# Kernel tuning notes

Measured on AMD Instinct MI355X. Metric: run time of the kernel, lower is better.

The kernel has to match this reference:

```python
import jax, jax.numpy as jnp
import numpy as np

A, C, H, W = 8, 256, 80, 108      # agents, channels, cf_h, cf_w from the module
NUM_CLASSES = 7
OUT_H, OUT_W = 256, 256


def warp_affine(feat, M):
    """Bilinear affine warp of feat [C,H,W] with sampling matrix M [2,3].
    dst(u,v) = src(M @ [u,v,1]); out-of-bounds samples are zero (kornia zero padding)."""
    c, h, w = feat.shape
    vs, us = jnp.meshgrid(jnp.arange(h, dtype=feat.dtype),
                          jnp.arange(w, dtype=feat.dtype), indexing='ij')
    sx = M[0, 0] * us + M[0, 1] * vs + M[0, 2]
    sy = M[1, 0] * us + M[1, 1] * vs + M[1, 2]
    x0 = jnp.floor(sx)
    y0 = jnp.floor(sy)
    wx = sx - x0
    wy = sy - y0
    x0i = x0.astype(jnp.int32)
    y0i = y0.astype(jnp.int32)

    def tap(yy, xx, wgt):
        valid = (yy >= 0) & (yy < h) & (xx >= 0) & (xx < w)
        yyc = jnp.clip(yy, 0, h - 1)
        xxc = jnp.clip(xx, 0, w - 1)
        return feat[:, yyc, xxc] * (wgt * valid)[None]

    return (tap(y0i, x0i, (1 - wy) * (1 - wx))
            + tap(y0i, x0i + 1, (1 - wy) * wx)
            + tap(y0i + 1, x0i, wy * (1 - wx))
            + tap(y0i + 1, x0i + 1, wy * wx))


def resize_bilinear_align_corners(img, oh, ow):
    """F.interpolate(..., mode='bilinear', align_corners=True) for img [N,C,H,W]."""
    h, w = img.shape[-2:]
    ys = jnp.linspace(0.0, h - 1.0, oh, dtype=img.dtype)
    xs = jnp.linspace(0.0, w - 1.0, ow, dtype=img.dtype)
    y0 = jnp.clip(jnp.floor(ys).astype(jnp.int32), 0, h - 2)
    x0 = jnp.clip(jnp.floor(xs).astype(jnp.int32), 0, w - 2)
    wy = (ys - y0)[None, None, :, None]
    wx = (xs - x0)[None, None, None, :]
    row = img[:, :, y0, :] * (1 - wy) + img[:, :, y0 + 1, :] * wy   # [N,C,oh,W]
    return row[:, :, :, x0] * (1 - wx) + row[:, :, :, x0 + 1] * wx  # [N,C,oh,ow]


def setup_inputs() -> dict:
    key = jax.random.key(0)
    k1, k2, k3, k4, k5, k6 = jax.random.split(key, 6)
    x = jax.random.normal(k1, (A, C, H, W), jnp.float32)
    # near-identity per-pair affine sampling matrices with small rotation/shear + translation
    rel = jnp.tile(jnp.eye(2, 3, dtype=jnp.float32), (A, A, 1, 1))
    rel = rel + 0.05 * jax.random.normal(k2, (A, A, 2, 3), jnp.float32)
    rel = rel.at[..., 2].add(10.0 * jax.random.normal(k3, (A, A, 2), jnp.float32))
    adjacency_matrix = jax.random.randint(k4, (A, A), 0, 2, dtype=jnp.int32)
    car_masks = jax.random.uniform(k5, (A, 256, 256), jnp.float32)
    w_cls = 0.02 * jax.random.normal(k6, (NUM_CLASSES, C), jnp.float32)
    b_cls = jnp.zeros((NUM_CLASSES,), jnp.float32)
    return {"x": x, "relative_tfs": rel, "adjacency_matrix": adjacency_matrix,
            "car_masks": car_masks, "w_cls": w_cls, "b_cls": b_cls}


def reference(x, relative_tfs, adjacency_matrix, car_masks, w_cls, b_cls):
    # x = x + F.interpolate(car_masks.unsqueeze(1), (cf_h, cf_w), 'bilinear')  (align_corners=False)
    cm = jax.image.resize(car_masks[:, None], (A, 1, H, W), method="bilinear")
    x = x + cm

    # aggregate_features: per ego-agent i, warp all agents' features into i's frame,
    # zero agents with adjacency[i,j]==0, and sum over j.
    warp_all = jax.vmap(warp_affine)                       # over agents j
    warped = jax.vmap(lambda Ms: warp_all(x, Ms))(relative_tfs)  # [A,A,C,H,W]
    fov = (adjacency_matrix != 0).astype(x.dtype)          # [A,A]
    aggr = jnp.einsum('ij,ijchw->ichw', fov, warped)       # masked sum over j

    def predict(f):  # mask_prediction (1x1 conv) + sigmoid
        logits = jnp.einsum('oc,achw->aohw', w_cls, f) + b_cls[None, :, None, None]
        return jax.nn.sigmoid(logits)

    solo_x = resize_bilinear_align_corners(predict(x), OUT_H, OUT_W)
    aggr_x = resize_bilinear_align_corners(predict(aggr), OUT_H, OUT_W)
    return (solo_x, aggr_x)
```

## Files before the change

kernel.cpp:

```cpp
#include <hip/hip_runtime.h>
#include <hip/hip_bf16.h>

#define A_N 8
#define C_N 256
#define H_N 80
#define W_N 108
#define P_N (H_N * W_N)
#define P4_N (P_N / 4)
#define O_N 7
#define MH 256
#define MW 256
#define OUT_HW 256
#define TPA 34

__device__ __forceinline__ float sigmoidf_(float zv) {
    return 1.0f / (1.0f + __expf(-zv));
}

__launch_bounds__(256)
__global__ void k_conv(const float* __restrict__ x, const float* __restrict__ masks,
                       const float* __restrict__ w, const float* __restrict__ b,
                       float* __restrict__ z, float* __restrict__ ssolo)
{
    __shared__ float4 s_red[4][64][O_N];
    __shared__ float  s_cm[256];

    const int tid = threadIdx.x;
    const int bi  = blockIdx.x;
    const int a   = bi / TPA;
    const int t   = bi - a * TPA;

    {
        const int ppx = t * 256 + tid;
        const int pc  = min(ppx, P_N - 1);
        const int oy = pc / W_N, ox = pc - oy * W_N;
        const float ksy = 256.0f / 80.0f;
        const float ksx = 256.0f / 108.0f;
        const float rky = 0.3125f;
        const float rkx = 0.421875f;
        const float sfy = ((float)oy + 0.5f) * ksy - 0.5f;
        const float sfx = ((float)ox + 0.5f) * ksx - 0.5f;
        const int iyS = (int)ceilf(sfy - ksy);
        const int ixS = (int)ceilf(sfx - ksx);

        float wxv[5];
        float wxs = 0.0f;
        #pragma unroll
        for (int q = 0; q < 5; ++q) {
            const int ix = ixS + q;
            float wv = fmaxf(0.0f, 1.0f - fabsf(sfx - (float)ix) * rkx);
            wv = (ix >= 0 && ix < MW) ? wv : 0.0f;
            wxv[q] = wv;
            wxs += wv;
        }
        const float* mp = masks + (size_t)a * (MH * MW);
        float acc = 0.0f, wys = 0.0f;
        #pragma unroll
        for (int r = 0; r < 7; ++r) {
            const int iy = iyS + r;
            float wy = fmaxf(0.0f, 1.0f - fabsf(sfy - (float)iy) * rky);
            wy = (iy >= 0 && iy < MH) ? wy : 0.0f;
            wys += wy;
            const float* row = mp + min(max(iy, 0), MH - 1) * MW;
            float rs = 0.0f;
            #pragma unroll
            for (int q = 0; q < 5; ++q)
                rs = fmaf(wxv[q], row[min(max(ixS + q, 0), MW - 1)], rs);
            acc = fmaf(wy, rs, acc);
        }
        s_cm[tid] = acc / (wys * wxs);
    }
    __syncthreads();

    const int wq   = tid >> 6;
    const int lane = tid & 63;
    const int px4  = t * 64 + lane;
    const int px4c = min(px4, P4_N - 1);

    const float4 cm4 = make_float4(s_cm[lane * 4], s_cm[lane * 4 + 1],
                                   s_cm[lane * 4 + 2], s_cm[lane * 4 + 3]);

    const float4* xp = reinterpret_cast<const float4*>(x)
                     + (size_t)(a * C_N + wq * 64) * P4_N + px4c;
    const float* wp = w + wq * 64;

    float4 acc[O_N];
    #pragma unroll
    for (int o = 0; o < O_N; ++o) acc[o] = make_float4(0.f, 0.f, 0.f, 0.f);

    float4 va[8], vb[8];

#define LOADB(buf, cb)                                            \
    _Pragma("unroll")                                             \
    for (int u = 0; u < 8; ++u) buf[u] = xp[(size_t)((cb) + u) * P4_N];

#define COMPB(buf, cb)                                            \
    _Pragma("unroll")                                             \
    for (int u = 0; u < 8; ++u) {                                 \
        float4 v = buf[u];                                        \
        v.x += cm4.x; v.y += cm4.y; v.z += cm4.z; v.w += cm4.w;   \
        _Pragma("unroll")                                         \
        for (int o = 0; o < O_N; ++o) {                           \
            const float wv = wp[o * C_N + (cb) + u];              \
            acc[o].x = fmaf(wv, v.x, acc[o].x);                   \
            acc[o].y = fmaf(wv, v.y, acc[o].y);                   \
            acc[o].z = fmaf(wv, v.z, acc[o].z);                   \
            acc[o].w = fmaf(wv, v.w, acc[o].w);                   \
        }                                                         \
    }

    LOADB(va, 0)
    LOADB(vb, 8)   COMPB(va, 0)
    LOADB(va, 16)  COMPB(vb, 8)
    LOADB(vb, 24)  COMPB(va, 16)
    LOADB(va, 32)  COMPB(vb, 24)
    LOADB(vb, 40)  COMPB(va, 32)
    LOADB(va, 48)  COMPB(vb, 40)
    LOADB(vb, 56)  COMPB(va, 48)
    COMPB(vb, 56)
#undef LOADB
#undef COMPB

    #pragma unroll
    for (int o = 0; o < O_N; ++o) s_red[wq][lane][o] = acc[o];
    __syncthreads();

    for (int pair = tid; pair < 64 * O_N; pair += 256) {
        const int pl = pair & 63;
        const int o  = pair >> 6;
        const int pg = t * 64 + pl;
        if (pg >= P4_N) continue;
        const float4 s0 = s_red[0][pl][o];
        const float4 s1 = s_red[1][pl][o];
        const float4 s2 = s_red[2][pl][o];
        const float4 s3 = s_red[3][pl][o];
        float4 zv;
        zv.x = s0.x + s1.x + s2.x + s3.x;
        zv.y = s0.y + s1.y + s2.y + s3.y;
        zv.z = s0.z + s1.z + s2.z + s3.z;
        zv.w = s0.w + s1.w + s2.w + s3.w;
        const float bo = b[o];
        const size_t ob = (size_t)(a * O_N + o) * P4_N + pg;
        reinterpret_cast<float4*>(z)[ob] = zv;
        float4 sv;
        sv.x = sigmoidf_(zv.x + bo);
        sv.y = sigmoidf_(zv.y + bo);
        sv.z = sigmoidf_(zv.z + bo);
        sv.w = sigmoidf_(zv.w + bo);
        reinterpret_cast<float4*>(ssolo)[ob] = sv;
    }
}

__launch_bounds__(64)
__global__ void k_aggr(const float* __restrict__ z, const float* __restrict__ rel,
                       const int* __restrict__ adj, const float* __restrict__ b,
                       float* __restrict__ saggr)
{
    const int i = blockIdx.x / 135;
    const int p = (blockIdx.x - i * 135) * 64 + threadIdx.x;
    const int vy = p / W_N, ux = p - vy * W_N;
    const float fu = (float)ux, fv = (float)vy;

    float acc[O_N];
    #pragma unroll
    for (int o = 0; o < O_N; ++o) acc[o] = b[o];

    for (int j = 0; j < A_N; ++j) {
        if (adj[i * A_N + j] == 0) continue;
        const float* M = rel + (i * A_N + j) * 6;
        float sx = M[0] * fu + M[1] * fv + M[2];
        float sy = M[3] * fu + M[4] * fv + M[5];
        if (!(sx > -1.0f && sx < (float)W_N && sy > -1.0f && sy < (float)H_N)) continue;
        float x0f = floorf(sx), y0f = floorf(sy);
        float wx = sx - x0f, wy = sy - y0f;
        int x0 = (int)x0f, y0 = (int)y0f;
        int x1 = x0 + 1,  y1 = y0 + 1;
        float w00 = (1.0f - wy) * (1.0f - wx), w01 = (1.0f - wy) * wx;
        float w10 = wy * (1.0f - wx),          w11 = wy * wx;
        if (x0 < 0)    { w00 = 0.0f; w10 = 0.0f; x0 = 0; }
        if (x1 >= W_N) { w01 = 0.0f; w11 = 0.0f; x1 = W_N - 1; }
        if (y0 < 0)    { w00 = 0.0f; w01 = 0.0f; y0 = 0; }
        if (y1 >= H_N) { w10 = 0.0f; w11 = 0.0f; y1 = H_N - 1; }
        const int i00 = y0 * W_N + x0, i01 = y0 * W_N + x1;
        const int i10 = y1 * W_N + x0, i11 = y1 * W_N + x1;
        const float* zj = z + j * O_N * P_N;
        #pragma unroll
        for (int o = 0; o < O_N; ++o) {
            const float* zp = zj + o * P_N;
            acc[o] += w00 * zp[i00] + w01 * zp[i01] + w10 * zp[i10] + w11 * zp[i11];
        }
    }
    const int ob = i * O_N * P_N + p;
    #pragma unroll
    for (int o = 0; o < O_N; ++o) saggr[ob + o * P_N] = sigmoidf_(acc[o]);
}

__launch_bounds__(256)
__global__ void k_upsample(const float* __restrict__ ssolo, const float* __restrict__ saggr,
                           float* __restrict__ out)
{
    const int idx = blockIdx.x * 256 + threadIdx.x;
    int k = idx;
    const int oxq = k & 63;   k >>= 6;
    const int oy  = k & 255;  k >>= 8;
    const int o   = k % O_N;  k /= O_N;
    const int a   = k & 7;    k >>= 3;
    const int t   = k;

    const float* src = (t == 0 ? ssolo : saggr) + (a * O_N + o) * P_N;
    float syf = (float)oy * (79.0f / 255.0f);
    int y0 = (int)syf; y0 = min(y0, H_N - 2);
    float wy = syf - (float)y0;
    const float* r0 = src + y0 * W_N;
    const float* r1 = r0 + W_N;

    float res[4];
    #pragma unroll
    for (int q = 0; q < 4; ++q) {
        int ox = oxq * 4 + q;
        float sxf = (float)ox * (107.0f / 255.0f);
        int x0 = (int)sxf; x0 = min(x0, W_N - 2);
        float wx = sxf - (float)x0;
        float c0 = r0[x0]     * (1.0f - wy) + r1[x0]     * wy;
        float c1 = r0[x0 + 1] * (1.0f - wy) + r1[x0 + 1] * wy;
        res[q] = c0 * (1.0f - wx) + c1 * wx;
    }
    *reinterpret_cast<float4*>(out + (size_t)idx * 4) =
        make_float4(res[0], res[1], res[2], res[3]);
}

extern "C" void kernel_launch(void* const* d_in, const int* in_sizes, int n_in,
                              void* d_out, int out_size, void* d_ws, size_t ws_size,
                              hipStream_t stream)
{
    (void)in_sizes; (void)n_in; (void)out_size; (void)ws_size;
    const float* x    = (const float*)d_in[0];
    const float* rel  = (const float*)d_in[1];
    const int*   adj  = (const int*)d_in[2];
    const float* cmsk = (const float*)d_in[3];
    const float* wcls = (const float*)d_in[4];
    const float* bcls = (const float*)d_in[5];
    float* out = (float*)d_out;

    float* ws    = (float*)d_ws;
    float* z     = ws;
    float* ssolo = z     + A_N * O_N * P_N;
    float* saggr = ssolo + A_N * O_N * P_N;

    k_conv    <<<A_N * TPA, 256, 0, stream>>>(x, cmsk, wcls, bcls, z, ssolo);
    k_aggr    <<<1080, 64, 0, stream>>>(z, rel, adj, bcls, saggr);
    k_upsample<<<7168, 256, 0, stream>>>(ssolo, saggr, out);
}
```

Before: 46.33 us.

## Stage 1x1-conv input through LDS with async global_load_lds double buffering

The channel-reduction loop in the conv kernel no longer keeps per-thread register double buffers of global float4 loads. It now streams 16-channel slabs into a double-buffered LDS tile using direct global-to-LDS loads, with manual vmcnt waits and barriers between stages. Weights are also preloaded into LDS in a padded layout, replacing repeated global reads. The aim is to cut register pressure and overlap memory with compute. The cost is two barriers per stage and a larger LDS footprint, and __launch_bounds__ is removed.

```diff
diff --git a/kernel.cpp b/kernel.cpp
--- a/kernel.cpp
+++ b/kernel.cpp
@@ -17,18 +17,26 @@
     return 1.0f / (1.0f + __expf(-zv));
 }
 
-__launch_bounds__(256)
 __global__ void k_conv(const float* __restrict__ x, const float* __restrict__ masks,
                        const float* __restrict__ w, const float* __restrict__ b,
                        float* __restrict__ z, float* __restrict__ ssolo)
 {
-    __shared__ float4 s_red[4][64][O_N];
-    __shared__ float  s_cm[256];
-
-    const int tid = threadIdx.x;
-    const int bi  = blockIdx.x;
-    const int a   = bi / TPA;
-    const int t   = bi - a * TPA;
+    __shared__ float s_x[8192];
+    __shared__ float s_w[2048];
+    __shared__ float s_cm[256];
+
+    const int tid  = threadIdx.x;
+    const int lane = tid & 63;
+    const int wid  = tid >> 6;
+    const int a    = blockIdx.x / TPA;
+    const int t    = blockIdx.x - a * TPA;
+
+    #pragma unroll
+    for (int k = 0; k < 8; ++k) {
+        const int idx = k * 256 + tid;
+        const int c = idx >> 3, o = idx & 7;
+        s_w[idx] = (o < O_N) ? w[o * C_N + c] : 0.0f;
+    }
 
     {
         const int ppx = t * 256 + tid;
@@ -54,7 +62,7 @@
             wxs += wv;
         }
         const float* mp = masks + (size_t)a * (MH * MW);
-        float acc = 0.0f, wys = 0.0f;
+        float acm = 0.0f, wys = 0.0f;
         #pragma unroll
         for (int r = 0; r < 7; ++r) {
             const int iy = iyS + r;
@@ -66,74 +74,88 @@
             #pragma unroll
             for (int q = 0; q < 5; ++q)
                 rs = fmaf(wxv[q], row[min(max(ixS + q, 0), MW - 1)], rs);
-            acc = fmaf(wy, rs, acc);
-        }
-        s_cm[tid] = acc / (wys * wxs);
+            acm = fmaf(wy, rs, acm);
+        }
+        s_cm[tid] = acm / (wys * wxs);
     }
     __syncthreads();
 
-    const int wq   = tid >> 6;
-    const int lane = tid & 63;
     const int px4  = t * 64 + lane;
     const int px4c = min(px4, P4_N - 1);
+    const float* xa = x + (size_t)a * C_N * P_N;
 
     const float4 cm4 = make_float4(s_cm[lane * 4], s_cm[lane * 4 + 1],
                                    s_cm[lane * 4 + 2], s_cm[lane * 4 + 3]);
 
-    const float4* xp = reinterpret_cast<const float4*>(x)
-                     + (size_t)(a * C_N + wq * 64) * P4_N + px4c;
-    const float* wp = w + wq * 64;
-
     float4 acc[O_N];
     #pragma unroll
     for (int o = 0; o < O_N; ++o) acc[o] = make_float4(0.f, 0.f, 0.f, 0.f);
 
-    float4 va[8], vb[8];
-
-#define LOADB(buf, cb)                                            \
-    _Pragma("unroll")                                             \
-    for (int u = 0; u < 8; ++u) buf[u] = xp[(size_t)((cb) + u) * P4_N];
-
-#define COMPB(buf, cb)                                            \
-    _Pragma("unroll")                                             \
-    for (int u = 0; u < 8; ++u) {                                 \
-        float4 v = buf[u];                                        \
-        v.x += cm4.x; v.y += cm4.y; v.z += cm4.z; v.w += cm4.w;   \
-        _Pragma("unroll")                                         \
-        for (int o = 0; o < O_N; ++o) {                           \
-            const float wv = wp[o * C_N + (cb) + u];              \
-            acc[o].x = fmaf(wv, v.x, acc[o].x);                   \
-            acc[o].y = fmaf(wv, v.y, acc[o].y);                   \
-            acc[o].z = fmaf(wv, v.z, acc[o].z);                   \
-            acc[o].w = fmaf(wv, v.w, acc[o].w);                   \
-        }                                                         \
-    }
-
-    LOADB(va, 0)
-    LOADB(vb, 8)   COMPB(va, 0)
-    LOADB(va, 16)  COMPB(vb, 8)
-    LOADB(vb, 24)  COMPB(va, 16)
-    LOADB(va, 32)  COMPB(vb, 24)
-    LOADB(vb, 40)  COMPB(va, 32)
-    LOADB(va, 48)  COMPB(vb, 40)
-    LOADB(vb, 56)  COMPB(va, 48)
-    COMPB(vb, 56)
-#undef LOADB
-#undef COMPB
-
-    #pragma unroll
-    for (int o = 0; o < O_N; ++o) s_red[wq][lane][o] = acc[o];
+#define STAGE(dstofs, step)                                                    \
+    { _Pragma("unroll")                                                        \
+      for (int r = 0; r < 4; ++r) {                                            \
+          const int c = (step) * 16 + r * 4 + wid;                             \
+          const float* gs = xa + (size_t)c * P4_N * 4 + (size_t)px4c * 4;      \
+          __builtin_amdgcn_global_load_lds(                                    \
+              (const __attribute__((address_space(1))) void*)gs,               \
+              (__attribute__((address_space(3))) void*)(s_x + (dstofs) + (r * 4 + wid) * 256), \
+              16, 0, 0);                                                       \
+      } }
+
+#define COMPS(srcofs, step)                                                    \
+    { _Pragma("unroll")                                                        \
+      for (int r = 0; r < 4; ++r) {                                            \
+          const int c = (step) * 16 + r * 4 + wid;                             \
+          float4 v = *reinterpret_cast<const float4*>(                         \
+                         s_x + (srcofs) + (r * 4 + wid) * 256 + lane * 4);     \
+          v.x += cm4.x; v.y += cm4.y; v.z += cm4.z; v.w += cm4.w;              \
+          const float* wc = s_w + c * 8;                                       \
+          _Pragma("unroll")                                                    \
+          for (int o = 0; o < O_N; ++o) {                                      \
+              const float wv = wc[o];                                          \
+              acc[o].x = fmaf(wv, v.x, acc[o].x);                              \
+              acc[o].y = fmaf(wv, v.y, acc[o].y);                              \
+              acc[o].z = fmaf(wv, v.z, acc[o].z);                              \
+              acc[o].w = fmaf(wv, v.w, acc[o].w);                              \
+          }                                                                    \
+      } }
+
+    STAGE(0, 0)
+    #pragma unroll
+    for (int s = 0; s < 16; ++s) {
+        const int bo = (s & 1) * 4096;
+        const int bn = ((s + 1) & 1) * 4096;
+        if (s < 15) {
+            STAGE(bn, s + 1)
+            asm volatile("s_waitcnt vmcnt(4)" ::: "memory");
+        } else {
+            asm volatile("s_waitcnt vmcnt(0)" ::: "memory");
+        }
+        __builtin_amdgcn_s_barrier();
+        __builtin_amdgcn_sched_barrier(0);
+        COMPS(bo, s)
+        asm volatile("" ::: "memory");
+        __builtin_amdgcn_s_barrier();
+    }
+#undef STAGE
+#undef COMPS
+
     __syncthreads();
+    float4* sred = reinterpret_cast<float4*>(s_x);
+    #pragma unroll
+    for (int o = 0; o < O_N; ++o)
+        sred[(wid * 64 + lane) * O_N + o] = acc[o];
+    __syncthreads();
 
     for (int pair = tid; pair < 64 * O_N; pair += 256) {
-        const int pl = pair & 63;
+        const int px = pair & 63;
         const int o  = pair >> 6;
-        const int pg = t * 64 + pl;
+        const int pg = t * 64 + px;
         if (pg >= P4_N) continue;
-        const float4 s0 = s_red[0][pl][o];
-        const float4 s1 = s_red[1][pl][o];
-        const float4 s2 = s_red[2][pl][o];
-        const float4 s3 = s_red[3][pl][o];
+        const float4 s0 = sred[(0 * 64 + px) * O_N + o];
+        const float4 s1 = sred[(1 * 64 + px) * O_N + o];
+        const float4 s2 = sred[(2 * 64 + px) * O_N + o];
+        const float4 s3 = sred[(3 * 64 + px) * O_N + o];
         float4 zv;
         zv.x = s0.x + s1.x + s2.x + s3.x;
         zv.y = s0.y + s1.y + s2.y + s3.y;
```

Result: slower. 79.20 us (+70.9%).
